# Kernel optimization log

Measured on AMD Instinct MI355X. Metric: run time of the kernel, lower is better.

The kernel has to match this reference:

```python
import jax, jax.numpy as jnp
import numpy as np

# Circuit dimensions (levelized DAG stand-in for the SDD-derived network)
B = 1024          # batch
NUM_VARS = 2048   # propositional variables
LEAVES = 2 * NUM_VARS  # positive + negative literal nodes (smooth circuit)
LEVELS = 12       # internal levels (topological depth)
WIDTH = 4096      # internal nodes per level
FANIN = 4         # children per internal node
TOTAL = LEAVES + LEVELS * WIDTH  # total nodes in execution order


def setup_inputs() -> dict:
    key = jax.random.key(0)
    x = jax.random.uniform(key, (B, NUM_VARS), dtype=jnp.float32)
    rng = np.random.default_rng(0)
    # child_idx[l, i, k]: index (into the global node-output buffer) of the
    # k-th child of node i at level l. DAG constraint: children must be
    # earlier nodes, i.e. index < LEAVES + l * WIDTH.
    child_idx = np.zeros((LEVELS, WIDTH, FANIN), dtype=np.int32)
    for l in range(LEVELS):
        cap = LEAVES + l * WIDTH
        child_idx[l] = rng.integers(0, cap, size=(WIDTH, FANIN), dtype=np.int32)
    # op_type: 0 -> AND node (product of children), 1 -> OR node (sum of children)
    op_type = rng.integers(0, 2, size=(LEVELS, WIDTH)).astype(np.int32)
    return {"x": x,
            "child_idx": jnp.asarray(child_idx),
            "op_type": jnp.asarray(op_type)}


def reference(x, child_idx, op_type):
    """Bottom-up evaluation of the levelized arithmetic circuit.

    x:         [B, NUM_VARS] literal probabilities
    child_idx: [LEVELS, WIDTH, FANIN] int32 child indices (constants)
    op_type:   [LEVELS, WIDTH] int32, 0=AND (prod), 1=OR (sum)
    Returns:   [B] root node output (last node in execution order).
    """
    b = x.shape[0]
    # Leaf (literal/prob node) outputs: [x, 1-x] -> [B, LEAVES]
    leaf = jnp.concatenate([x, 1.0 - x], axis=1)
    buf = jnp.zeros((b, TOTAL), dtype=x.dtype)
    buf = buf.at[:, :LEAVES].set(leaf)
    n_levels = child_idx.shape[0]
    for l in range(n_levels):  # structural loop over circuit depth (small, fixed)
        ch = buf[:, child_idx[l]]                 # gather children: [B, WIDTH, FANIN]
        out = jnp.where(op_type[l] == 0,
                        jnp.prod(ch, axis=-1),    # AND nodes
                        jnp.sum(ch, axis=-1))     # OR nodes
        start = LEAVES + l * WIDTH
        buf = buf.at[:, start:start + WIDTH].set(out)
    return buf[:, -1]  # root output
```

## Files before the change

### kernel.cpp

```cpp
#include <hip/hip_runtime.h>

#define BATCH    1024
#define NUM_VARS 2048
#define LEAVES   (2 * NUM_VARS)
#define LEVELS   12
#define WIDTH    4096
#define TOTAL    (LEAVES + LEVELS * WIDTH)
#define NWORDS   (TOTAL / 32)

#define CAP      2048
#define BSLICE   4
#define NEVB     (BATCH / BSLICE)
#define ETHR     1024

#define ROWS     (NUM_VARS + CAP)
#define LDSTRIDE 4100

#define OFF_BUF   0
#define SZ_BUF    (4 * LDSTRIDE * 4)
#define OFF_ENC   (OFF_BUF + SZ_BUF)
#define SZ_ENC    (CAP * 16)
#define OFF_FLG   (OFF_ENC + SZ_ENC)
#define SZ_FLG    (NWORDS * 4)
#define OFF_NID   (OFF_FLG + SZ_FLG)
#define SZ_NID    ((CAP + 8) * 4)
#define OFF_MISC  (OFF_NID + SZ_NID)
#define SMEM_BYTES (OFF_MISC + 128)


__global__ __launch_bounds__(ETHR) void fused_kernel(const float* __restrict__ x,
                                                     const int4* __restrict__ child4,
                                                     const int*  __restrict__ op_type,
                                                     float* __restrict__ out)
{
    extern __shared__ char smem[];
    float*        buf      = (float*)(smem + OFF_BUF);
    int4*         enc_s    = (int4*)(smem + OFF_ENC);
    unsigned int* flg      = (unsigned int*)(smem + OFF_FLG);
    int*          nid      = (int*)(smem + OFF_NID);
    int*          lvl_cnt  = (int*)(smem + OFF_MISC);
    int*          lvl_base = lvl_cnt + LEVELS;
    int*          total_s  = lvl_base + LEVELS;

    const int tid  = threadIdx.x;
    const int lane = tid & 63;
    const int wv   = tid >> 6;

    const int pc_ = tid >> 8;
    const int pq  = tid & 255;
    const float4* xr4 =
        (const float4*)(x + (size_t)(blockIdx.x * BSLICE + pc_) * NUM_VARS);
    const float4 lf0 = xr4[pq];
    const float4 lf1 = xr4[pq + 256];

    for (int i = tid; i < NWORDS; i += ETHR)
        flg[i] = (i == NWORDS - 1) ? 0x80000000u : 0u;
    __syncthreads();

    for (int l = LEVELS - 1; l >= 0; --l) {
        const int wbase = 128 * (l + 1);
        const unsigned int fw = flg[wbase + (tid >> 3)];
        const int sh = (tid & 7) * 4;
        #pragma unroll
        for (int j = 0; j < 4; ++j) {
            if ((fw >> (sh + j)) & 1u) {
                const int4 c = child4[l * WIDTH + ((tid << 2) | j)];
                atomicOr(&flg[c.x >> 5], 1u << (c.x & 31));
                atomicOr(&flg[c.y >> 5], 1u << (c.y & 31));
                atomicOr(&flg[c.z >> 5], 1u << (c.z & 31));
                atomicOr(&flg[c.w >> 5], 1u << (c.w & 31));
            }
        }
        __syncthreads();
    }

    if (wv < LEVELS) {
        const unsigned int w0 = flg[128 * (wv + 1) + 2 * lane];
        const unsigned int w1 = flg[128 * (wv + 1) + 2 * lane + 1];
        const int pc = __popc(w0) + __popc(w1);
        int scan = pc;
        for (int d = 1; d < 64; d <<= 1) {
            const int up = __shfl_up(scan, d, 64);
            if (lane >= d) scan += up;
        }
        if (lane == 63) lvl_cnt[wv] = scan;
    }
    __syncthreads();
    if (tid == 0) {
        int s = 0;
        for (int l = 0; l < LEVELS; ++l) { lvl_base[l] = s; s += lvl_cnt[l]; }
        *total_s = (s < CAP) ? s : CAP;
    }
    __syncthreads();

    if (wv < LEVELS) {
        const unsigned int w0 = flg[128 * (wv + 1) + 2 * lane];
        const unsigned int w1 = flg[128 * (wv + 1) + 2 * lane + 1];
        const int pc = __popc(w0) + __popc(w1);
        int scan = pc;
        for (int d = 1; d < 64; d <<= 1) {
            const int up = __shfl_up(scan, d, 64);
            if (lane >= d) scan += up;
        }
        int base = lvl_base[wv] + scan - pc;
        const int nd0 = LEAVES + wv * WIDTH + 64 * lane;
        unsigned int w = w0;
        while (w) { const int b = __ffs(w) - 1; w &= w - 1;
                    if (base < CAP) nid[base] = nd0 + b;      base++; }
        w = w1;
        while (w) { const int b = __ffs(w) - 1; w &= w - 1;
                    if (base < CAP) nid[base] = nd0 + 32 + b; base++; }
    }
    __syncthreads();

    const int S = *total_s;
    for (int slot = tid; slot < S; slot += ETHR) {
        const int nd = nid[slot];
        const int4 c = child4[nd - LEAVES];
        const int  o = op_type[nd - LEAVES];
        int lo0 = 0, lo1 = 0, lo2 = 0, lo3 = 0;
        int hi0 = S, hi1 = S, hi2 = S, hi3 = S;
        #pragma unroll
        for (int it = 0; it < 11; ++it) {
            const int m0 = (lo0 + hi0) >> 1, m1 = (lo1 + hi1) >> 1;
            const int m2 = (lo2 + hi2) >> 1, m3 = (lo3 + hi3) >> 1;
            const int n0 = nid[m0], n1 = nid[m1], n2 = nid[m2], n3 = nid[m3];
            if (lo0 < hi0) { if (n0 < c.x) lo0 = m0 + 1; else hi0 = m0; }
            if (lo1 < hi1) { if (n1 < c.y) lo1 = m1 + 1; else hi1 = m1; }
            if (lo2 < hi2) { if (n2 < c.z) lo2 = m2 + 1; else hi2 = m2; }
            if (lo3 < hi3) { if (n3 < c.w) lo3 = m3 + 1; else hi3 = m3; }
        }
        int4 e;
        e.x = (c.x < NUM_VARS) ? c.x : (c.x < LEAVES) ? ((c.x - NUM_VARS) | 0x4000)
                                                      : (NUM_VARS + lo0);
        e.y = (c.y < NUM_VARS) ? c.y : (c.y < LEAVES) ? ((c.y - NUM_VARS) | 0x4000)
                                                      : (NUM_VARS + lo1);
        e.z = (c.z < NUM_VARS) ? c.z : (c.z < LEAVES) ? ((c.z - NUM_VARS) | 0x4000)
                                                      : (NUM_VARS + lo2);
        e.w = (c.w < NUM_VARS) ? c.w : (c.w < LEAVES) ? ((c.w - NUM_VARS) | 0x4000)
                                                      : (NUM_VARS + lo3);
        e.x |= o << 20;
        enc_s[slot] = e;
    }

    {
        float* br = buf + pc_ * LDSTRIDE;
        ((float4*)br)[pq]       = lf0;
        ((float4*)br)[pq + 256] = lf1;
    }
    __syncthreads();

    const int col = tid & 3;
    const int nl  = tid >> 2;
    float* bc = buf + col * LDSTRIDE;

    for (int l = 0; l < LEVELS; ++l) {
        const int n  = lvl_cnt[l];
        const int sb = lvl_base[l];
        for (int i = nl; i < n; i += ETHR / BSLICE) {
            const int4 e = enc_s[sb + i];
            float v0 = bc[e.x & 0x3FFF];
            float v1 = bc[e.y & 0x3FFF];
            float v2 = bc[e.z & 0x3FFF];
            float v3 = bc[e.w & 0x3FFF];
            v0 = (e.x & 0x4000) ? 1.0f - v0 : v0;
            v1 = (e.y & 0x4000) ? 1.0f - v1 : v1;
            v2 = (e.z & 0x4000) ? 1.0f - v2 : v2;
            v3 = (e.w & 0x4000) ? 1.0f - v3 : v3;
            const float p = ((v0 * v1) * v2) * v3;
            const float s = ((v0 + v1) + v2) + v3;
            const float r = (e.x & (1 << 20)) ? s : p;
            bc[NUM_VARS + sb + i] = r;
            if (l == LEVELS - 1 && i == n - 1)
                out[blockIdx.x * BSLICE + col] = r;
        }
        __syncthreads();
    }
}

extern "C" void kernel_launch(void* const* d_in, const int* in_sizes, int n_in,
                              void* d_out, int out_size, void* d_ws, size_t ws_size,
                              hipStream_t stream)
{
    const float* x       = (const float*)d_in[0];
    const int4*  child4  = (const int4*)d_in[1];
    const int*   op_type = (const int*)d_in[2];
    float*       out     = (float*)d_out;
    (void)d_ws; (void)ws_size;

    static bool lds_opted = false;
    if (!lds_opted) {
        hipFuncSetAttribute((const void*)fused_kernel,
                            hipFuncAttributeMaxDynamicSharedMemorySize, SMEM_BYTES);
        lds_opted = true;
    }

    fused_kernel<<<NEVB, ETHR, SMEM_BYTES, stream>>>(x, child4, op_type, out);
}
```

Measured before the change: 76.38 us.

## Replace binary-search compaction with per-word prefix ranks, prefetch child table

Node-to-slot mapping during compaction now comes from a per-word prefix-base table in LDS plus a popcount of the liveness bitmap, replacing an 11-step binary search over the node-id list for each child. Each block also warms the L2 with a slice of the child table. The four child loads in the backward liveness pass are issued unconditionally, using a dummy index when a node is not live, so they can overlap. The leaf staging into LDS moves earlier to overlap with flag initialisation. The cost is extra LDS for the scan table and some wasted global loads.

```diff
diff --git a/kernel.cpp b/kernel.cpp
--- a/kernel.cpp
+++ b/kernel.cpp
@@ -7,6 +7,7 @@
 #define WIDTH    4096
 #define TOTAL    (LEAVES + LEVELS * WIDTH)
 #define NWORDS   (TOTAL / 32)
+#define NNWORDS  (NWORDS - 128)
 
 #define CAP      2048
 #define BSLICE   4
@@ -24,8 +25,12 @@
 #define SZ_FLG    (NWORDS * 4)
 #define OFF_NID   (OFF_FLG + SZ_FLG)
 #define SZ_NID    ((CAP + 8) * 4)
-#define OFF_MISC  (OFF_NID + SZ_NID)
+#define OFF_WSC   (OFF_NID + SZ_NID)
+#define SZ_WSC    (NNWORDS * 4)
+#define OFF_MISC  (OFF_WSC + SZ_WSC)
 #define SMEM_BYTES (OFF_MISC + 128)
+
+#define WARM_N   1536
 
 
 __global__ __launch_bounds__(ETHR) void fused_kernel(const float* __restrict__ x,
@@ -38,6 +43,7 @@
     int4*         enc_s    = (int4*)(smem + OFF_ENC);
     unsigned int* flg      = (unsigned int*)(smem + OFF_FLG);
     int*          nid      = (int*)(smem + OFF_NID);
+    int*          wscan    = (int*)(smem + OFF_WSC);
     int*          lvl_cnt  = (int*)(smem + OFF_MISC);
     int*          lvl_base = lvl_cnt + LEVELS;
     int*          total_s  = lvl_base + LEVELS;
@@ -52,24 +58,62 @@
         (const float4*)(x + (size_t)(blockIdx.x * BSLICE + pc_) * NUM_VARS);
     const float4 lf0 = xr4[pq];
     const float4 lf1 = xr4[pq + 256];
+    {
+        const int seg = (blockIdx.x >> 3) & 31;
+        const int4 w0 = child4[seg * WARM_N + tid];
+        int acc = w0.x ^ w0.y ^ w0.z ^ w0.w;
+        if (tid < WARM_N - 1024) {
+            const int4 w1 = child4[seg * WARM_N + 1024 + tid];
+            acc ^= w1.x ^ w1.y ^ w1.z ^ w1.w;
+        }
+        asm volatile("" :: "v"(acc));
+    }
 
     for (int i = tid; i < NWORDS; i += ETHR)
         flg[i] = (i == NWORDS - 1) ? 0x80000000u : 0u;
+
+    {
+        float* br = buf + pc_ * LDSTRIDE;
+        ((float4*)br)[pq]       = lf0;
+        ((float4*)br)[pq + 256] = lf1;
+    }
     __syncthreads();
 
     for (int l = LEVELS - 1; l >= 0; --l) {
         const int wbase = 128 * (l + 1);
         const unsigned int fw = flg[wbase + (tid >> 3)];
         const int sh = (tid & 7) * 4;
-        #pragma unroll
-        for (int j = 0; j < 4; ++j) {
-            if ((fw >> (sh + j)) & 1u) {
-                const int4 c = child4[l * WIDTH + ((tid << 2) | j)];
-                atomicOr(&flg[c.x >> 5], 1u << (c.x & 31));
-                atomicOr(&flg[c.y >> 5], 1u << (c.y & 31));
-                atomicOr(&flg[c.z >> 5], 1u << (c.z & 31));
-                atomicOr(&flg[c.w >> 5], 1u << (c.w & 31));
-            }
+        int4 c0, c1, c2, c3;
+        {
+            const int b = l * WIDTH + (tid << 2);
+            c0 = child4[((fw >> (sh + 0)) & 1u) ? b + 0 : 0];
+            c1 = child4[((fw >> (sh + 1)) & 1u) ? b + 1 : 0];
+            c2 = child4[((fw >> (sh + 2)) & 1u) ? b + 2 : 0];
+            c3 = child4[((fw >> (sh + 3)) & 1u) ? b + 3 : 0];
+        }
+        if ((fw >> (sh + 0)) & 1u) {
+            atomicOr(&flg[c0.x >> 5], 1u << (c0.x & 31));
+            atomicOr(&flg[c0.y >> 5], 1u << (c0.y & 31));
+            atomicOr(&flg[c0.z >> 5], 1u << (c0.z & 31));
+            atomicOr(&flg[c0.w >> 5], 1u << (c0.w & 31));
+        }
+        if ((fw >> (sh + 1)) & 1u) {
+            atomicOr(&flg[c1.x >> 5], 1u << (c1.x & 31));
+            atomicOr(&flg[c1.y >> 5], 1u << (c1.y & 31));
+            atomicOr(&flg[c1.z >> 5], 1u << (c1.z & 31));
+            atomicOr(&flg[c1.w >> 5], 1u << (c1.w & 31));
+        }
+        if ((fw >> (sh + 2)) & 1u) {
+            atomicOr(&flg[c2.x >> 5], 1u << (c2.x & 31));
+            atomicOr(&flg[c2.y >> 5], 1u << (c2.y & 31));
+            atomicOr(&flg[c2.z >> 5], 1u << (c2.z & 31));
+            atomicOr(&flg[c2.w >> 5], 1u << (c2.w & 31));
+        }
+        if ((fw >> (sh + 3)) & 1u) {
+            atomicOr(&flg[c3.x >> 5], 1u << (c3.x & 31));
+            atomicOr(&flg[c3.y >> 5], 1u << (c3.y & 31));
+            atomicOr(&flg[c3.z >> 5], 1u << (c3.z & 31));
+            atomicOr(&flg[c3.w >> 5], 1u << (c3.w & 31));
         }
         __syncthreads();
     }
@@ -103,6 +147,8 @@
             if (lane >= d) scan += up;
         }
         int base = lvl_base[wv] + scan - pc;
+        wscan[128 * wv + 2 * lane]     = base;
+        wscan[128 * wv + 2 * lane + 1] = base + __popc(w0);
         const int nd0 = LEAVES + wv * WIDTH + 64 * lane;
         unsigned int w = w0;
         while (w) { const int b = __ffs(w) - 1; w &= w - 1;
@@ -118,35 +164,38 @@
         const int nd = nid[slot];
         const int4 c = child4[nd - LEAVES];
         const int  o = op_type[nd - LEAVES];
-        int lo0 = 0, lo1 = 0, lo2 = 0, lo3 = 0;
-        int hi0 = S, hi1 = S, hi2 = S, hi3 = S;
-        #pragma unroll
-        for (int it = 0; it < 11; ++it) {
-            const int m0 = (lo0 + hi0) >> 1, m1 = (lo1 + hi1) >> 1;
-            const int m2 = (lo2 + hi2) >> 1, m3 = (lo3 + hi3) >> 1;
-            const int n0 = nid[m0], n1 = nid[m1], n2 = nid[m2], n3 = nid[m3];
-            if (lo0 < hi0) { if (n0 < c.x) lo0 = m0 + 1; else hi0 = m0; }
-            if (lo1 < hi1) { if (n1 < c.y) lo1 = m1 + 1; else hi1 = m1; }
-            if (lo2 < hi2) { if (n2 < c.z) lo2 = m2 + 1; else hi2 = m2; }
-            if (lo3 < hi3) { if (n3 < c.w) lo3 = m3 + 1; else hi3 = m3; }
-        }
         int4 e;
-        e.x = (c.x < NUM_VARS) ? c.x : (c.x < LEAVES) ? ((c.x - NUM_VARS) | 0x4000)
-                                                      : (NUM_VARS + lo0);
-        e.y = (c.y < NUM_VARS) ? c.y : (c.y < LEAVES) ? ((c.y - NUM_VARS) | 0x4000)
-                                                      : (NUM_VARS + lo1);
-        e.z = (c.z < NUM_VARS) ? c.z : (c.z < LEAVES) ? ((c.z - NUM_VARS) | 0x4000)
-                                                      : (NUM_VARS + lo2);
-        e.w = (c.w < NUM_VARS) ? c.w : (c.w < LEAVES) ? ((c.w - NUM_VARS) | 0x4000)
-                                                      : (NUM_VARS + lo3);
+        {
+            const int cc = c.x;
+            const int w  = cc >> 5;
+            const int r  = (cc >= LEAVES)
+                ? NUM_VARS + wscan[w - 128] + __popc(flg[w] & ((1u << (cc & 31)) - 1))
+                : (cc < NUM_VARS ? cc : (cc - NUM_VARS) | 0x4000);
+            e.x = r;
+        }
+        {
+            const int cc = c.y;
+            const int w  = cc >> 5;
+            e.y = (cc >= LEAVES)
+                ? NUM_VARS + wscan[w - 128] + __popc(flg[w] & ((1u << (cc & 31)) - 1))
+                : (cc < NUM_VARS ? cc : (cc - NUM_VARS) | 0x4000);
+        }
+        {
+            const int cc = c.z;
+            const int w  = cc >> 5;
+            e.z = (cc >= LEAVES)
+                ? NUM_VARS + wscan[w - 128] + __popc(flg[w] & ((1u << (cc & 31)) - 1))
+                : (cc < NUM_VARS ? cc : (cc - NUM_VARS) | 0x4000);
+        }
+        {
+            const int cc = c.w;
+            const int w  = cc >> 5;
+            e.w = (cc >= LEAVES)
+                ? NUM_VARS + wscan[w - 128] + __popc(flg[w] & ((1u << (cc & 31)) - 1))
+                : (cc < NUM_VARS ? cc : (cc - NUM_VARS) | 0x4000);
+        }
         e.x |= o << 20;
         enc_s[slot] = e;
-    }
-
-    {
-        float* br = buf + pc_ * LDSTRIDE;
-        ((float4*)br)[pq]       = lf0;
-        ((float4*)br)[pq + 256] = lf1;
     }
     __syncthreads();
 
```

Result: no change. 75.35 us (-1.3%).
